# Kernel tuning notes

Hardware: AMD Instinct MI355X
Metric: run time of the kernel (lower is better)

## Reference

```python
import jax, jax.numpy as jnp
import numpy as np

N_NODES = 50000
HEADS1 = 4
NEG_SLOPE = 0.2
EPS = 1e-16


def gat_conv(x, edge_index, W, att_src, att_dst, bias, heads, out_ch, concat):
    # edge_index: [2, E] with self-loops already appended by caller
    src, dst = edge_index[0], edge_index[1]
    N = x.shape[0]
    h = (x @ W).reshape(N, heads, out_ch)                      # [N, H, C]
    a_src = jnp.sum(h * att_src, axis=-1)                      # [N, H]
    a_dst = jnp.sum(h * att_dst, axis=-1)                      # [N, H]
    e = a_src[src] + a_dst[dst]                                # [E, H]
    e = jnp.where(e > 0, e, NEG_SLOPE * e)                     # leaky_relu
    m = jax.ops.segment_max(e, dst, num_segments=N)            # [N, H]
    alpha = jnp.exp(e - m[dst])                                # [E, H]
    denom = jax.ops.segment_sum(alpha, dst, num_segments=N)    # [N, H]
    alpha = alpha / (denom[dst] + EPS)                         # [E, H]
    msg = alpha[:, :, None] * h[src]                           # [E, H, C]
    out = jax.ops.segment_sum(msg, dst, num_segments=N)        # [N, H, C]
    if concat:
        out = out.reshape(N, heads * out_ch)
    else:
        out = out.mean(axis=1)
    return out + bias, alpha


def setup_inputs() -> dict:
    key = jax.random.key(0)
    ks = jax.random.split(key, 12)
    N, F, H, heads, C, E = N_NODES, 256, 64, HEADS1, 40, 800000
    g = 0.1
    return {
        "x": jax.random.normal(ks[0], (N, F), dtype=jnp.float32),
        "edge_index": jax.random.randint(ks[1], (2, E), 0, N, dtype=jnp.int32),
        "W1": jax.random.normal(ks[2], (F, heads * H), dtype=jnp.float32) * g,
        "att_src1": jax.random.normal(ks[3], (heads, H), dtype=jnp.float32) * g,
        "att_dst1": jax.random.normal(ks[4], (heads, H), dtype=jnp.float32) * g,
        "b1": jnp.zeros((heads * H,), dtype=jnp.float32),
        "W2": jax.random.normal(ks[5], (heads * H, C), dtype=jnp.float32) * g,
        "att_src2": jax.random.normal(ks[6], (1, C), dtype=jnp.float32) * g,
        "att_dst2": jax.random.normal(ks[7], (1, C), dtype=jnp.float32) * g,
        "b2": jnp.zeros((C,), dtype=jnp.float32),
    }


def reference(x, edge_index, W1, att_src1, att_dst1, b1, W2, att_src2, att_dst2, b2):
    N = x.shape[0]
    # add self-loops (PyG GATConv default)
    loops = jnp.arange(N, dtype=edge_index.dtype)
    ei = jnp.concatenate([edge_index, jnp.stack([loops, loops])], axis=1)
    # dropout is identity in eval mode
    h1, alpha = gat_conv(x, ei, W1, att_src1, att_dst1, b1,
                         HEADS1, W1.shape[1] // HEADS1, concat=True)
    h1 = jax.nn.elu(h1)
    h2, _ = gat_conv(h1, ei, W2, att_src2, att_dst2, b2,
                     1, W2.shape[1], concat=False)
    return jax.nn.log_softmax(h2, axis=1), alpha
```

## Files before the change

### kernel.cpp

```cpp
#include <hip/hip_runtime.h>
#include <math.h>

#define N_NODES 50000
#define HC1 256
#define H1 4
#define C2 40
#define C2P 64
#define E0 800000
#define ET 850000
#define NEG_SLOPE 0.2f
#define EPS_A 1e-16f

typedef __bf16 bf16x8 __attribute__((ext_vector_type(8)));
typedef float f32x4 __attribute__((ext_vector_type(4)));
typedef unsigned short u16x8 __attribute__((ext_vector_type(8)));


__device__ inline unsigned short f2bf(float f) {
    unsigned u = __float_as_uint(f);
    return (unsigned short)((u + 0x7FFFu + ((u >> 16) & 1u)) >> 16);
}
__device__ inline float bf_lo(unsigned q) { return __uint_as_float(q << 16); }
__device__ inline float bf_hi(unsigned q) { return __uint_as_float(q & 0xFFFF0000u); }


__device__ inline int edge_src(const int* __restrict__ ei, int e) {
    return (e < E0) ? ei[e] : (e - E0);
}
__device__ inline int edge_dst(const int* __restrict__ ei, int e) {
    return (e < E0) ? ei[E0 + e] : (e - E0);
}

__device__ inline void acc8(float ac[8], float A, uint4 q) {
    ac[0] += A * bf_lo(q.x); ac[1] += A * bf_hi(q.x);
    ac[2] += A * bf_lo(q.y); ac[3] += A * bf_hi(q.y);
    ac[4] += A * bf_lo(q.z); ac[5] += A * bf_hi(q.z);
    ac[6] += A * bf_lo(q.w); ac[7] += A * bf_hi(q.w);
}

__device__ inline float leaky(float v) { return v > 0.f ? v : NEG_SLOPE * v; }


#define CV_X 3200000
#define CV_W1 65536
#define CV_W2 16384
#define CV_TOT (CV_X + CV_W1 + CV_W2 + N_NODES)

__global__ void convert_all_kernel(const float* __restrict__ x,
                                   const float* __restrict__ W1,
                                   const float* __restrict__ W2,
                                   ushort4* __restrict__ xbf,
                                   unsigned short* __restrict__ w1t,
                                   unsigned short* __restrict__ w2t,
                                   int* __restrict__ deg) {
    int tid = blockIdx.x * blockDim.x + threadIdx.x;
    if (tid < CV_X) {
        float4 v = ((const float4*)x)[tid];
        ushort4 w;
        w.x = f2bf(v.x); w.y = f2bf(v.y); w.z = f2bf(v.z); w.w = f2bf(v.w);
        xbf[tid] = w;
    } else if (tid < CV_X + CV_W1) {
        int i = tid - CV_X;
        int n = i >> 8, k = i & 255;
        w1t[i] = f2bf(W1[k * 256 + n]);
    } else if (tid < CV_X + CV_W1 + CV_W2) {
        int i = tid - CV_X - CV_W1;
        int n = i >> 8, k = i & 255;
        w2t[i] = (n < C2) ? f2bf(W2[k * C2 + n]) : (unsigned short)0;
    } else if (tid < CV_TOT) {
        deg[tid - CV_X - CV_W1 - CV_W2] = 0;
    }
}


__global__ void hist_kernel(const int* __restrict__ ei, int* __restrict__ deg) {
    int e = blockIdx.x * blockDim.x + threadIdx.x;
    if (e >= ET) return;
    atomicAdd(&deg[edge_dst(ei, e)], 1);
}

__global__ __launch_bounds__(256) void scan_block_kernel(const int* __restrict__ deg,
                                                         int* __restrict__ excl,
                                                         int* __restrict__ bsum) {
    __shared__ int tmp[256];
    int t = threadIdx.x;
    int i = blockIdx.x * 256 + t;
    int v = (i < N_NODES) ? deg[i] : 0;
    tmp[t] = v;
    __syncthreads();
#pragma unroll
    for (int o = 1; o < 256; o <<= 1) {
        int x = (t >= o) ? tmp[t - o] : 0;
        __syncthreads();
        tmp[t] += x;
        __syncthreads();
    }
    if (i < N_NODES) excl[i] = tmp[t] - v;
    if (t == 255) bsum[blockIdx.x] = tmp[255];
}

#define NSCAN_B 196

__global__ __launch_bounds__(256) void scan_top_kernel(int* __restrict__ bsum) {
    __shared__ int tmp[256];
    int t = threadIdx.x;
    int v = (t < NSCAN_B) ? bsum[t] : 0;
    tmp[t] = v;
    __syncthreads();
#pragma unroll
    for (int o = 1; o < 256; o <<= 1) {
        int x = (t >= o) ? tmp[t - o] : 0;
        __syncthreads();
        tmp[t] += x;
        __syncthreads();
    }
    if (t < NSCAN_B) bsum[t] = tmp[t] - v;
}

__global__ __launch_bounds__(256) void scan_add_kernel(int* __restrict__ offsets,
                                                       int* __restrict__ cursor,
                                                       const int* __restrict__ bsum) {
    int i = blockIdx.x * 256 + threadIdx.x;
    if (i < N_NODES) {
        int v = offsets[i] + bsum[blockIdx.x];
        offsets[i] = v;
        cursor[i] = v;
    }
    if (i == 0) offsets[N_NODES] = ET;
}

__global__ void scatter_kernel(const int* __restrict__ ei, int* __restrict__ cursor,
                               int2* __restrict__ csr_es) {
    int e = blockIdx.x * blockDim.x + threadIdx.x;
    if (e >= ET) return;
    int d = edge_dst(ei, e);
    int pos = atomicAdd(&cursor[d], 1);
    csr_es[pos] = make_int2(e, edge_src(ei, e));
}


template <int TBM, int TBN, int WROWS, int WCOLS>
__global__ __launch_bounds__(256) void gemm_mfma_kernel(const unsigned short* __restrict__ Abf,
                                                        const unsigned short* __restrict__ Bt,
                                                        unsigned short* __restrict__ Cbf,
                                                        const float* __restrict__ att_s,
                                                        const float* __restrict__ att_d,
                                                        float* __restrict__ a_src_o,
                                                        float* __restrict__ a_dst_o,
                                                        int M, int Nc, int attN, int hstride) {
    static_assert(TBM == WROWS * 64 && TBN == WCOLS * 64, "tile");
    constexpr int LDK = 40;
    __shared__ alignas(16) unsigned short As[TBM * LDK];
    __shared__ alignas(16) unsigned short Bs[TBN * LDK];
    const int t = threadIdx.x;
    const int lane = t & 63;
    const int w = t >> 6;
    const int quad = lane >> 4;
    const int l16 = lane & 15;
    const int wm = (w / WCOLS) * 64;
    const int wn = (w % WCOLS) * 64;
    const int bm = blockIdx.x * TBM;
    const int bn = blockIdx.y * TBN;

    f32x4 acc[4][4] = {};

    for (int k0 = 0; k0 < 256; k0 += 32) {
        __syncthreads();
#pragma unroll
        for (int i = 0; i < TBM / 64; ++i) {
            int idx = t + i * 256;
            int row = idx >> 2, seg = idx & 3;
            u16x8 v = {};
            if (bm + row < M)
                v = *(const u16x8*)(Abf + (size_t)(bm + row) * 256 + k0 + seg * 8);
            *(u16x8*)&As[row * LDK + seg * 8] = v;
        }
#pragma unroll
        for (int i = 0; i < TBN / 64; ++i) {
            int idx = t + i * 256;
            int row = idx >> 2, seg = idx & 3;
            u16x8 v = *(const u16x8*)(Bt + (size_t)(bn + row) * 256 + k0 + seg * 8);
            *(u16x8*)&Bs[row * LDK + seg * 8] = v;
        }
        __syncthreads();

        bf16x8 af[4], bfr[4];
#pragma unroll
        for (int mi = 0; mi < 4; ++mi)
            af[mi] = *(const bf16x8*)&As[(wm + mi * 16 + l16) * LDK + quad * 8];
#pragma unroll
        for (int ni = 0; ni < 4; ++ni)
            bfr[ni] = *(const bf16x8*)&Bs[(wn + ni * 16 + l16) * LDK + quad * 8];
#pragma unroll
        for (int mi = 0; mi < 4; ++mi)
#pragma unroll
            for (int ni = 0; ni < 4; ++ni)
                acc[mi][ni] = __builtin_amdgcn_mfma_f32_16x16x32_bf16(
                    af[mi], bfr[ni], acc[mi][ni], 0, 0, 0);
    }

#pragma unroll
    for (int mi = 0; mi < 4; ++mi)
#pragma unroll
        for (int ni = 0; ni < 4; ++ni)
#pragma unroll
            for (int r = 0; r < 4; ++r) {
                int row = bm + wm + mi * 16 + quad * 4 + r;
                int col = bn + wn + ni * 16 + l16;
                if (row < M)
                    Cbf[(size_t)row * Nc + col] = f2bf(acc[mi][ni][r]);
            }

    float asc[4], adc[4];
#pragma unroll
    for (int ni = 0; ni < 4; ++ni) {
        int col = bn + wn + ni * 16 + l16;
        bool valid = col < attN;
        asc[ni] = valid ? att_s[col] : 0.f;
        adc[ni] = valid ? att_d[col] : 0.f;
    }
    float vs[16], vd[16];
#pragma unroll
    for (int mi = 0; mi < 4; ++mi)
#pragma unroll
        for (int r = 0; r < 4; ++r) {
            float s = 0.f, dd = 0.f;
#pragma unroll
            for (int ni = 0; ni < 4; ++ni) {
                s += acc[mi][ni][r] * asc[ni];
                dd += acc[mi][ni][r] * adc[ni];
            }
            vs[mi * 4 + r] = s;
            vd[mi * 4 + r] = dd;
        }
#pragma unroll
    for (int k = 0; k < 4; ++k) {
        const int o = 1 << k;
        const int b = (l16 >> k) & 1;
#pragma unroll
        for (int j = 0; j < (8 >> k); ++j) {
            float lo = vs[2 * j], hi = vs[2 * j + 1];
            float keep = b ? hi : lo, send = b ? lo : hi;
            vs[j] = keep + __shfl_xor(send, o);
            lo = vd[2 * j]; hi = vd[2 * j + 1];
            keep = b ? hi : lo; send = b ? lo : hi;
            vd[j] = keep + __shfl_xor(send, o);
        }
    }
    {
        int mi = l16 >> 2, r = l16 & 3;
        int row = bm + wm + mi * 16 + quad * 4 + r;
        int head = (bn + wn) >> 6;
        if (row < M) {
            a_src_o[(size_t)row * hstride + head] = vs[0];
            a_dst_o[(size_t)row * hstride + head] = vd[0];
        }
    }
}


__global__ __launch_bounds__(256) void l1_fused_kernel(const int* __restrict__ off,
                                                       const int2* __restrict__ csr_es,
                                                       const float4* __restrict__ a_src4,
                                                       const float4* __restrict__ a_dst4,
                                                       const unsigned* __restrict__ h1bf,
                                                       const float* __restrict__ b1,
                                                       float4* __restrict__ alpha_out4,
                                                       unsigned* __restrict__ out1bf) {
    __shared__ int    s_w[4][2][32];
    __shared__ float4 p_w[4][2][32];
    int t = threadIdx.x;
    int w = t >> 6, lane = t & 63;
    int half = lane >> 5, li = lane & 31;
    int d = blockIdx.x * 8 + w * 2 + half;
    int beg = off[d], end = off[d + 1];
    int deg = end - beg;
    int nch = (deg + 31) >> 5;
    int cnt0 = min(deg, 32);
    bool act0 = li < cnt0;
    float4 ad4 = a_dst4[d];
    int headc = li >> 3;

    float ac[8] = {};
    float4 sum = make_float4(0.f, 0.f, 0.f, 0.f);
    float4 mx = make_float4(-INFINITY, -INFINITY, -INFINITY, -INFINITY);
    int2 es0 = make_int2(0, 0);
    float4 p0 = make_float4(0.f, 0.f, 0.f, 0.f);

    const float* aw = (const float*)&p_w[w][half][0];
    const int*   sw = &s_w[w][half][0];

    if (nch == 1) {
        float4 l0 = make_float4(-INFINITY, -INFINITY, -INFINITY, -INFINITY);
        if (act0) {
            es0 = csr_es[beg + li];
            float4 as4 = a_src4[es0.y];
            l0.x = leaky(as4.x + ad4.x);
            l0.y = leaky(as4.y + ad4.y);
            l0.z = leaky(as4.z + ad4.z);
            l0.w = leaky(as4.w + ad4.w);
            s_w[w][half][li] = es0.y;
        }
        mx = l0;
#pragma unroll
        for (int o = 1; o <= 16; o <<= 1) {
            mx.x = fmaxf(mx.x, __shfl_xor(mx.x, o));
            mx.y = fmaxf(mx.y, __shfl_xor(mx.y, o));
            mx.z = fmaxf(mx.z, __shfl_xor(mx.z, o));
            mx.w = fmaxf(mx.w, __shfl_xor(mx.w, o));
        }
        p0.x = __expf(l0.x - mx.x);
        p0.y = __expf(l0.y - mx.y);
        p0.z = __expf(l0.z - mx.z);
        p0.w = __expf(l0.w - mx.w);
        if (act0) p_w[w][half][li] = p0;
        sum = p0;
        int j = 0;
        for (; j + 3 < cnt0; j += 4) {
            int s0 = sw[j], s1 = sw[j + 1], s2 = sw[j + 2], s3 = sw[j + 3];
            float A0 = aw[4 * j + headc],       A1 = aw[4 * (j + 1) + headc];
            float A2 = aw[4 * (j + 2) + headc], A3 = aw[4 * (j + 3) + headc];
            uint4 q0 = *(const uint4*)&h1bf[(unsigned)s0 * 128u + 4u * li];
            uint4 q1 = *(const uint4*)&h1bf[(unsigned)s1 * 128u + 4u * li];
            uint4 q2 = *(const uint4*)&h1bf[(unsigned)s2 * 128u + 4u * li];
            uint4 q3 = *(const uint4*)&h1bf[(unsigned)s3 * 128u + 4u * li];
            acc8(ac, A0, q0); acc8(ac, A1, q1);
            acc8(ac, A2, q2); acc8(ac, A3, q3);
        }
        for (; j < cnt0; ++j) {
            int s = sw[j];
            float A = aw[4 * j + headc];
            uint4 q = *(const uint4*)&h1bf[(unsigned)s * 128u + 4u * li];
            acc8(ac, A, q);
        }
    } else {
        for (int cc = 0; cc < nch; ++cc) {
            int idx = beg + cc * 32 + li;
            if (idx < end) {
                int2 es = csr_es[idx];
                float4 as4 = a_src4[es.y];
                mx.x = fmaxf(mx.x, leaky(as4.x + ad4.x));
                mx.y = fmaxf(mx.y, leaky(as4.y + ad4.y));
                mx.z = fmaxf(mx.z, leaky(as4.z + ad4.z));
                mx.w = fmaxf(mx.w, leaky(as4.w + ad4.w));
            }
        }
#pragma unroll
        for (int o = 1; o <= 16; o <<= 1) {
            mx.x = fmaxf(mx.x, __shfl_xor(mx.x, o));
            mx.y = fmaxf(mx.y, __shfl_xor(mx.y, o));
            mx.z = fmaxf(mx.z, __shfl_xor(mx.z, o));
            mx.w = fmaxf(mx.w, __shfl_xor(mx.w, o));
        }
        for (int cc = 0; cc < nch; ++cc) {
            int idx = beg + cc * 32 + li;
            if (idx < end) {
                int2 es = csr_es[idx];
                float4 as4 = a_src4[es.y];
                sum.x += __expf(leaky(as4.x + ad4.x) - mx.x);
                sum.y += __expf(leaky(as4.y + ad4.y) - mx.y);
                sum.z += __expf(leaky(as4.z + ad4.z) - mx.z);
                sum.w += __expf(leaky(as4.w + ad4.w) - mx.w);
            }
        }
    }

#pragma unroll
    for (int o = 1; o <= 16; o <<= 1) {
        sum.x += __shfl_xor(sum.x, o);
        sum.y += __shfl_xor(sum.y, o);
        sum.z += __shfl_xor(sum.z, o);
        sum.w += __shfl_xor(sum.w, o);
    }
    float4 inv;
    inv.x = 1.f / (sum.x + EPS_A); inv.y = 1.f / (sum.y + EPS_A);
    inv.z = 1.f / (sum.z + EPS_A); inv.w = 1.f / (sum.w + EPS_A);
    float invh = (headc == 0) ? inv.x : (headc == 1) ? inv.y
               : (headc == 2) ? inv.z : inv.w;

    if (nch == 1) {
        if (act0) {
            float4 al0;
            al0.x = p0.x * inv.x; al0.y = p0.y * inv.y;
            al0.z = p0.z * inv.z; al0.w = p0.w * inv.w;
            alpha_out4[es0.x] = al0;
        }
    } else {
        for (int cc = 0; cc < nch; ++cc) {
            int idx = beg + cc * 32 + li;
            int cnt = min(32, deg - cc * 32);
            if (idx < end) {
                int2 es = csr_es[idx];
                float4 as4 = a_src4[es.y];
                float4 p;
                p.x = __expf(leaky(as4.x + ad4.x) - mx.x);
                p.y = __expf(leaky(as4.y + ad4.y) - mx.y);
                p.z = __expf(leaky(as4.z + ad4.z) - mx.z);
                p.w = __expf(leaky(as4.w + ad4.w) - mx.w);
                float4 al;
                al.x = p.x * inv.x; al.y = p.y * inv.y;
                al.z = p.z * inv.z; al.w = p.w * inv.w;
                alpha_out4[es.x] = al;
                s_w[w][half][li] = es.y;
                p_w[w][half][li] = p;
            }
            for (int j = 0; j < cnt; ++j) {
                int s = sw[j];
                float A = aw[4 * j + headc];
                uint4 q = *(const uint4*)&h1bf[(unsigned)s * 128u + 4u * li];
                acc8(ac, A, q);
            }
        }
    }

#pragma unroll
    for (int c = 0; c < 8; ++c) ac[c] *= invh;

    float4 bb0 = *(const float4*)&b1[8 * li];
    float4 bb1 = *(const float4*)&b1[8 * li + 4];
    float v0 = ac[0] + bb0.x, v1 = ac[1] + bb0.y;
    float v2 = ac[2] + bb0.z, v3 = ac[3] + bb0.w;
    float v4 = ac[4] + bb1.x, v5 = ac[5] + bb1.y;
    float v6 = ac[6] + bb1.z, v7 = ac[7] + bb1.w;
    v0 = v0 > 0.f ? v0 : __expf(v0) - 1.f;
    v1 = v1 > 0.f ? v1 : __expf(v1) - 1.f;
    v2 = v2 > 0.f ? v2 : __expf(v2) - 1.f;
    v3 = v3 > 0.f ? v3 : __expf(v3) - 1.f;
    v4 = v4 > 0.f ? v4 : __expf(v4) - 1.f;
    v5 = v5 > 0.f ? v5 : __expf(v5) - 1.f;
    v6 = v6 > 0.f ? v6 : __expf(v6) - 1.f;
    v7 = v7 > 0.f ? v7 : __expf(v7) - 1.f;
    uint4 qo;
    qo.x = ((unsigned)f2bf(v1) << 16) | (unsigned)f2bf(v0);
    qo.y = ((unsigned)f2bf(v3) << 16) | (unsigned)f2bf(v2);
    qo.z = ((unsigned)f2bf(v5) << 16) | (unsigned)f2bf(v4);
    qo.w = ((unsigned)f2bf(v7) << 16) | (unsigned)f2bf(v6);
    *(uint4*)&out1bf[(size_t)d * 128 + 4 * li] = qo;
}


__global__ __launch_bounds__(256) void l2_fused_kernel(const int* __restrict__ off,
                                                       const int2* __restrict__ csr_es,
                                                       const float* __restrict__ a_src,
                                                       const float* __restrict__ a_dst,
                                                       const unsigned* __restrict__ h2bf,
                                                       const float* __restrict__ b2,
                                                       float* __restrict__ out) {
    __shared__ uint2 sp_w[4][2][32];
    int t = threadIdx.x;
    int w = t >> 6, lane = t & 63;
    int half = lane >> 5, li = lane & 31;
    int d = blockIdx.x * 8 + w * 2 + half;
    int beg = off[d], end = off[d + 1];
    int deg = end - beg;
    float ad = a_dst[d];
    int nch = (deg + 31) >> 5;
    int cnt0 = min(deg, 32);
    bool act0 = li < cnt0;

    float sum = 0.f, acc0 = 0.f, acc1 = 0.f;

    if (nch == 1) {
        float el0 = -INFINITY; int s0 = 0;
        if (act0) {
            int2 es = csr_es[beg + li];
            s0 = es.y;
            el0 = leaky(a_src[s0] + ad);
        }
        float mx = el0;
#pragma unroll
        for (int o = 1; o <= 16; o <<= 1) mx = fmaxf(mx, __shfl_xor(mx, o));
        float p0 = __expf(el0 - mx);
        if (act0) sp_w[w][half][li] = make_uint2((unsigned)s0, __float_as_uint(p0));
        sum = p0;
        int j = 0;
        for (; j + 3 < cnt0; j += 4) {
            uint2 e0 = sp_w[w][half][j],     e1 = sp_w[w][half][j + 1];
            uint2 e2 = sp_w[w][half][j + 2], e3 = sp_w[w][half][j + 3];
            float A0 = __uint_as_float(e0.y), A1 = __uint_as_float(e1.y);
            float A2 = __uint_as_float(e2.y), A3 = __uint_as_float(e3.y);
            unsigned q0 = h2bf[e0.x * 32u + li];
            unsigned q1 = h2bf[e1.x * 32u + li];
            unsigned q2 = h2bf[e2.x * 32u + li];
            unsigned q3 = h2bf[e3.x * 32u + li];
            acc0 += A0 * bf_lo(q0) + A1 * bf_lo(q1);
            acc1 += A0 * bf_hi(q0) + A1 * bf_hi(q1);
            acc0 += A2 * bf_lo(q2) + A3 * bf_lo(q3);
            acc1 += A2 * bf_hi(q2) + A3 * bf_hi(q3);
        }
        for (; j < cnt0; ++j) {
            uint2 e0 = sp_w[w][half][j];
            float A0 = __uint_as_float(e0.y);
            unsigned q = h2bf[e0.x * 32u + li];
            acc0 += A0 * bf_lo(q);
            acc1 += A0 * bf_hi(q);
        }
    } else {
        float mx = -INFINITY;
        for (int cc = 0; cc < nch; ++cc) {
            int idx = beg + cc * 32 + li;
            if (idx < end) {
                int2 es = csr_es[idx];
                mx = fmaxf(mx, leaky(a_src[es.y] + ad));
            }
        }
#pragma unroll
        for (int o = 1; o <= 16; o <<= 1) mx = fmaxf(mx, __shfl_xor(mx, o));
        for (int cc = 0; cc < nch; ++cc) {
            int idx = beg + cc * 32 + li;
            int cnt = min(32, deg - cc * 32);
            if (idx < end) {
                int2 es = csr_es[idx];
                float el = leaky(a_src[es.y] + ad);
                float p = __expf(el - mx);
                sum += p;
                sp_w[w][half][li] = make_uint2((unsigned)es.y, __float_as_uint(p));
            }
            for (int j = 0; j < cnt; ++j) {
                uint2 e0 = sp_w[w][half][j];
                float A0 = __uint_as_float(e0.y);
                unsigned q = h2bf[e0.x * 32u + li];
                acc0 += A0 * bf_lo(q);
                acc1 += A0 * bf_hi(q);
            }
        }
    }

#pragma unroll
    for (int o = 1; o <= 16; o <<= 1) sum += __shfl_xor(sum, o);
    float inv = 1.f / (sum + EPS_A);
    acc0 *= inv;
    acc1 *= inv;

    bool act = li < 20;
    float v0 = act ? acc0 + b2[2 * li]     : -INFINITY;
    float v1 = act ? acc1 + b2[2 * li + 1] : -INFINITY;
    float mmx = fmaxf(v0, v1);
#pragma unroll
    for (int o = 16; o; o >>= 1) mmx = fmaxf(mmx, __shfl_xor(mmx, o));
    float ex = act ? __expf(v0 - mmx) + __expf(v1 - mmx) : 0.f;
#pragma unroll
    for (int o = 16; o; o >>= 1) ex += __shfl_xor(ex, o);
    float ls = __logf(ex);
    if (act)
        *(float2*)&out[(size_t)d * C2 + 2 * li] = make_float2(v0 - mmx - ls, v1 - mmx - ls);
}


extern "C" void kernel_launch(void* const* d_in, const int* in_sizes, int n_in,
                              void* d_out, int out_size, void* d_ws, size_t ws_size,
                              hipStream_t stream) {
    const float* x   = (const float*)d_in[0];
    const int*   ei  = (const int*)d_in[1];
    const float* W1  = (const float*)d_in[2];
    const float* as1 = (const float*)d_in[3];
    const float* ad1 = (const float*)d_in[4];
    const float* b1  = (const float*)d_in[5];
    const float* W2  = (const float*)d_in[6];
    const float* as2 = (const float*)d_in[7];
    const float* ad2 = (const float*)d_in[8];
    const float* b2  = (const float*)d_in[9];

    float* out   = (float*)d_out;
    float* alpha = out + (size_t)N_NODES * C2;

    unsigned* u32    = (unsigned*)d_ws;
    unsigned* h1bf   = u32;
    unsigned* xbf    = h1bf + 6400000;
    unsigned* h2bf   = xbf + 6400000;
    unsigned* w1t    = h2bf + 1600000;
    unsigned* w2t    = w1t + 32768;
    float* a_src1    = (float*)(w2t + 8192);
    float* a_dst1    = a_src1 + 200000;
    float* a_src2    = a_dst1 + 200000;
    float* a_dst2    = a_src2 + 50000;
    int*   deg       = (int*)(a_dst2 + 50000);
    int*   offs      = deg + 50000;
    int*   cursor    = offs + 50001;
    int*   bsum      = cursor + 50000;
    int2*  csr_es    = (int2*)(bsum + 257);
    unsigned* out1bf = xbf;

    const int TB = 256;
    const int EB = (ET + TB - 1) / TB;

    convert_all_kernel<<<(CV_TOT + TB - 1) / TB, TB, 0, stream>>>(
        x, W1, W2, (ushort4*)xbf, (unsigned short*)w1t, (unsigned short*)w2t, deg);

    hist_kernel<<<EB, TB, 0, stream>>>(ei, deg);
    scan_block_kernel<<<NSCAN_B, TB, 0, stream>>>(deg, offs, bsum);
    scan_top_kernel<<<1, TB, 0, stream>>>(bsum);
    scan_add_kernel<<<NSCAN_B, TB, 0, stream>>>(offs, cursor, bsum);
    scatter_kernel<<<EB, TB, 0, stream>>>(ei, cursor, csr_es);

    gemm_mfma_kernel<128, 128, 2, 2><<<dim3((N_NODES + 127) / 128, 2), TB, 0, stream>>>(
        (const unsigned short*)xbf, (const unsigned short*)w1t, (unsigned short*)h1bf,
        as1, ad1, a_src1, a_dst1, N_NODES, HC1, 256, H1);
    l1_fused_kernel<<<N_NODES / 8, TB, 0, stream>>>(offs, csr_es,
                                                    (const float4*)a_src1,
                                                    (const float4*)a_dst1,
                                                    h1bf, b1, (float4*)alpha, out1bf);

    gemm_mfma_kernel<256, 64, 4, 1><<<dim3((N_NODES + 255) / 256, 1), TB, 0, stream>>>(
        (const unsigned short*)out1bf, (const unsigned short*)w2t, (unsigned short*)h2bf,
        as2, ad2, a_src2, a_dst2, N_NODES, C2P, C2, 1);
    l2_fused_kernel<<<N_NODES / 8, TB, 0, stream>>>(offs, csr_es, a_src2, a_dst2,
                                                    h2bf, b2, out);
}
```

Before: 354.7 us.

## Prefetch gathered neighbor features before softmax with double-buffered register queues

In both fused aggregation kernels, the single-chunk path now broadcasts source indices by wavefront shuffle instead of through shared memory. It issues the first gathers of neighbor feature rows before the max/exp softmax reduction, so gather latency overlaps that work. The accumulation loop becomes a two-slot register double buffer of 4-edge groups, loading the next group while the current one is multiplied and accumulated. Edges past the degree are padded with index 0 and a zero weight, so every group processes exactly 4 edges. This adds extra loads for padded lanes and more register pressure.

```diff
diff --git a/kernel.cpp b/kernel.cpp
--- a/kernel.cpp
+++ b/kernel.cpp
@@ -259,6 +259,20 @@
 }
 
 
+#define L1_LOADQ(q, jb)                                                         \
+    _Pragma("unroll")                                                           \
+    for (int k = 0; k < 4; ++k) {                                               \
+        int s_ = __shfl(esy, shbase + (jb) + k);                                \
+        q[k] = *(const uint4*)&h1bf[(unsigned)s_ * 128u + 4u * li];             \
+    }
+
+#define L1_FMAQ(q, jb)                                                          \
+    _Pragma("unroll")                                                           \
+    for (int k = 0; k < 4; ++k) {                                               \
+        float A_ = aw[4 * ((jb) + k) + headc];                                  \
+        acc8(ac, A_, q[k]);                                                     \
+    }
+
 __global__ __launch_bounds__(256) void l1_fused_kernel(const int* __restrict__ off,
                                                        const int2* __restrict__ csr_es,
                                                        const float4* __restrict__ a_src4,
@@ -272,6 +286,7 @@
     int t = threadIdx.x;
     int w = t >> 6, lane = t & 63;
     int half = lane >> 5, li = lane & 31;
+    int shbase = half << 5;
     int d = blockIdx.x * 8 + w * 2 + half;
     int beg = off[d], end = off[d + 1];
     int deg = end - beg;
@@ -292,14 +307,23 @@
 
     if (nch == 1) {
         float4 l0 = make_float4(-INFINITY, -INFINITY, -INFINITY, -INFINITY);
+        float4 as4 = make_float4(0.f, 0.f, 0.f, 0.f);
         if (act0) {
             es0 = csr_es[beg + li];
-            float4 as4 = a_src4[es0.y];
+            as4 = a_src4[es0.y];
+        }
+        int esy = es0.y;
+        const int B = (cnt0 + 3) >> 2;
+
+        uint4 qa[4], qb[4];
+        L1_LOADQ(qa, 0);
+        if (B > 1) { L1_LOADQ(qb, 4); }
+
+        if (act0) {
             l0.x = leaky(as4.x + ad4.x);
             l0.y = leaky(as4.y + ad4.y);
             l0.z = leaky(as4.z + ad4.z);
             l0.w = leaky(as4.w + ad4.w);
-            s_w[w][half][li] = es0.y;
         }
         mx = l0;
 #pragma unroll
@@ -313,26 +337,17 @@
         p0.y = __expf(l0.y - mx.y);
         p0.z = __expf(l0.z - mx.z);
         p0.w = __expf(l0.w - mx.w);
-        if (act0) p_w[w][half][li] = p0;
+        p_w[w][half][li] = p0;
         sum = p0;
-        int j = 0;
-        for (; j + 3 < cnt0; j += 4) {
-            int s0 = sw[j], s1 = sw[j + 1], s2 = sw[j + 2], s3 = sw[j + 3];
-            float A0 = aw[4 * j + headc],       A1 = aw[4 * (j + 1) + headc];
-            float A2 = aw[4 * (j + 2) + headc], A3 = aw[4 * (j + 3) + headc];
-            uint4 q0 = *(const uint4*)&h1bf[(unsigned)s0 * 128u + 4u * li];
-            uint4 q1 = *(const uint4*)&h1bf[(unsigned)s1 * 128u + 4u * li];
-            uint4 q2 = *(const uint4*)&h1bf[(unsigned)s2 * 128u + 4u * li];
-            uint4 q3 = *(const uint4*)&h1bf[(unsigned)s3 * 128u + 4u * li];
-            acc8(ac, A0, q0); acc8(ac, A1, q1);
-            acc8(ac, A2, q2); acc8(ac, A3, q3);
-        }
-        for (; j < cnt0; ++j) {
-            int s = sw[j];
-            float A = aw[4 * j + headc];
-            uint4 q = *(const uint4*)&h1bf[(unsigned)s * 128u + 4u * li];
-            acc8(ac, A, q);
-        }
+
+        int i = 0;
+        for (; i + 2 <= B; i += 2) {
+            L1_FMAQ(qa, i * 4);
+            if (i + 2 < B) { L1_LOADQ(qa, (i + 2) * 4); }
+            L1_FMAQ(qb, i * 4 + 4);
+            if (i + 3 < B) { L1_LOADQ(qb, (i + 3) * 4); }
+        }
+        if (i < B) { L1_FMAQ(qa, i * 4); }
     } else {
         for (int cc = 0; cc < nch; ++cc) {
             int idx = beg + cc * 32 + li;
@@ -439,6 +454,21 @@
 }
 
 
+#define L2_LOADQ(q, jb)                                                         \
+    _Pragma("unroll")                                                           \
+    for (int k = 0; k < 4; ++k) {                                               \
+        int s_ = __shfl(s0, shbase + (jb) + k);                                 \
+        q[k] = h2bf[(unsigned)s_ * 32u + li];                                   \
+    }
+
+#define L2_FMAQ(q, jb)                                                          \
+    _Pragma("unroll")                                                           \
+    for (int k = 0; k < 4; ++k) {                                               \
+        float A_ = __shfl(p0, shbase + (jb) + k);                               \
+        acc0 += A_ * bf_lo(q[k]);                                               \
+        acc1 += A_ * bf_hi(q[k]);                                               \
+    }
+
 __global__ __launch_bounds__(256) void l2_fused_kernel(const int* __restrict__ off,
                                                        const int2* __restrict__ csr_es,
                                                        const float* __restrict__ a_src,
@@ -450,6 +480,7 @@
     int t = threadIdx.x;
     int w = t >> 6, lane = t & 63;
     int half = lane >> 5, li = lane & 31;
+    int shbase = half << 5;
     int d = blockIdx.x * 8 + w * 2 + half;
     int beg = off[d], end = off[d + 1];
     int deg = end - beg;
@@ -459,6 +490,7 @@
     bool act0 = li < cnt0;
 
     float sum = 0.f, acc0 = 0.f, acc1 = 0.f;
+    float p0 = 0.f;
 
     if (nch == 1) {
         float el0 = -INFINITY; int s0 = 0;
@@ -467,34 +499,25 @@
             s0 = es.y;
             el0 = leaky(a_src[s0] + ad);
         }
+        const int B = (cnt0 + 3) >> 2;
+        unsigned qa[4], qb[4];
+        L2_LOADQ(qa, 0);
+        if (B > 1) { L2_LOADQ(qb, 4); }
+
         float mx = el0;
 #pragma unroll
         for (int o = 1; o <= 16; o <<= 1) mx = fmaxf(mx, __shfl_xor(mx, o));
-        float p0 = __expf(el0 - mx);
-        if (act0) sp_w[w][half][li] = make_uint2((unsigned)s0, __float_as_uint(p0));
+        p0 = __expf(el0 - mx);
         sum = p0;
-        int j = 0;
-        for (; j + 3 < cnt0; j += 4) {
-            uint2 e0 = sp_w[w][half][j],     e1 = sp_w[w][half][j + 1];
-            uint2 e2 = sp_w[w][half][j + 2], e3 = sp_w[w][half][j + 3];
-            float A0 = __uint_as_float(e0.y), A1 = __uint_as_float(e1.y);
-            float A2 = __uint_as_float(e2.y), A3 = __uint_as_float(e3.y);
-            unsigned q0 = h2bf[e0.x * 32u + li];
-            unsigned q1 = h2bf[e1.x * 32u + li];
-            unsigned q2 = h2bf[e2.x * 32u + li];
-            unsigned q3 = h2bf[e3.x * 32u + li];
-            acc0 += A0 * bf_lo(q0) + A1 * bf_lo(q1);
-            acc1 += A0 * bf_hi(q0) + A1 * bf_hi(q1);
-            acc0 += A2 * bf_lo(q2) + A3 * bf_lo(q3);
-            acc1 += A2 * bf_hi(q2) + A3 * bf_hi(q3);
-        }
-        for (; j < cnt0; ++j) {
-            uint2 e0 = sp_w[w][half][j];
-            float A0 = __uint_as_float(e0.y);
-            unsigned q = h2bf[e0.x * 32u + li];
-            acc0 += A0 * bf_lo(q);
-            acc1 += A0 * bf_hi(q);
-        }
+
+        int i = 0;
+        for (; i + 2 <= B; i += 2) {
+            L2_FMAQ(qa, i * 4);
+            if (i + 2 < B) { L2_LOADQ(qa, (i + 2) * 4); }
+            L2_FMAQ(qb, i * 4 + 4);
+            if (i + 3 < B) { L2_LOADQ(qb, (i + 3) * 4); }
+        }
+        if (i < B) { L2_FMAQ(qa, i * 4); }
     } else {
         float mx = -INFINITY;
         for (int cc = 0; cc < nch; ++cc) {
```

Measured after the change: 358.9 us. Within noise of the previous version (+1.2%).
